# Optimization experiments

Hardware: AMD Instinct MI355X
Metric: run time of the kernel (lower is better)

The kernel has to match this reference:

```python
import jax, jax.numpy as jnp
import numpy as np

H = 1024          # hidden_dim
E = 8             # num_experts
TOP_K = 2
FF = 4 * H        # ExpertFFN inner dim (standard transformer FFN assumption)
B, S = 2, 2048


def setup_inputs() -> dict:
    key = jax.random.key(0)
    ks = jax.random.split(key, 12)
    std = 0.02 / np.sqrt(H)
    return {
        "x": jax.random.normal(ks[0], (B, S, H), dtype=jnp.float32),
        "gate_w": jax.random.normal(ks[1], (E, H), dtype=jnp.float32) * std,  # nn.Linear weight [out,in]
        "gate_b": jnp.zeros((E,), dtype=jnp.float32),                          # self.bias param
        # routed experts, stacked: FFN = W2 @ gelu(W1 @ x + b1) + b2
        "w1": jax.random.normal(ks[2], (E, H, FF), dtype=jnp.float32) * (1.0 / np.sqrt(H)),
        "b1": jnp.zeros((E, FF), dtype=jnp.float32),
        "w2": jax.random.normal(ks[3], (E, FF, H), dtype=jnp.float32) * (1.0 / np.sqrt(FF)),
        "b2": jnp.zeros((E, H), dtype=jnp.float32),
        # shared expert
        "sw1": jax.random.normal(ks[4], (H, FF), dtype=jnp.float32) * (1.0 / np.sqrt(H)),
        "sb1": jnp.zeros((FF,), dtype=jnp.float32),
        "sw2": jax.random.normal(ks[5], (FF, H), dtype=jnp.float32) * (1.0 / np.sqrt(FF)),
        "sb2": jnp.zeros((H,), dtype=jnp.float32),
    }


def _moe_forward(x, gate_w, gate_b, w1, b1, w2, b2, sw1, sb1, sw2, sb2):
    b, s, h = x.shape
    xf = x.reshape(-1, h)                                    # [T, H]
    # sigmoid gating with learned bias (aux-loss-free load balancing bias)
    scores = jax.nn.sigmoid(xf @ gate_w.T + gate_b)          # [T, E]
    top_scores, top_idx = jax.lax.top_k(scores, TOP_K)       # [T, k]
    top_scores = top_scores / (top_scores.sum(-1, keepdims=True) + 1e-6)
    # per-expert combine weights: sum of normalized scores over top-k slots
    comb = (jax.nn.one_hot(top_idx, E, dtype=xf.dtype) * top_scores[..., None]).sum(1)  # [T, E]
    # dense grouped FFN over all experts (reference; faithful math to masked dispatch)
    hdn = jax.nn.gelu(jnp.einsum('th,ehf->etf', xf, w1) + b1[:, None, :], approximate=False)
    y = jnp.einsum('etf,efh->eth', hdn, w2) + b2[:, None, :]  # [E, T, H]
    routed = jnp.einsum('te,eth->th', comb, y)                # [T, H]
    shared = (jax.nn.gelu(xf @ sw1 + sb1, approximate=False) @ sw2 + sb2) * 0.1
    return (routed + shared).reshape(b, s, h)                 # dropout: eval mode (identity)


def reference(x, gate_w, gate_b, w1, b1, w2, b2, sw1, sb1, sw2, sb2):
    return _moe_forward(x, gate_w, gate_b, w1, b1, w2, b2, sw1, sb1, sw2, sb2)
```

## Files before the change

### kernel.cpp

```cpp
#include <hip/hip_runtime.h>
#include <stdint.h>

#define H_DIM 1024
#define E_NUM 8
#define FF_DIM 4096
#define T_TOK 4096
#define MAX_MT 104

typedef __bf16 bf16x8 __attribute__((ext_vector_type(8)));
typedef float f32x4 __attribute__((ext_vector_type(4)));

#define AS1 __attribute__((address_space(1)))
#define AS3 __attribute__((address_space(3)))

__device__ __forceinline__ unsigned short f2bf(float f) {
  union { float f; uint32_t u; } v; v.f = f;
  uint32_t u = v.u;
  uint32_t r = u + 0x7fffu + ((u >> 16) & 1u);
  return (unsigned short)(r >> 16);
}

__device__ __forceinline__ float gelu_f(float x) {
  float s = x * x;
  float g = x * (1.5957691216f + 0.0713548162f * s);
  float t = __expf(-g);
  return x * __builtin_amdgcn_rcpf(1.0f + t);
}

__global__ __launch_bounds__(64) void gate_kernel(
    const float* __restrict__ x, const float* __restrict__ gw, const float* __restrict__ gb,
    int* __restrict__ topidx, float* __restrict__ topw, int* __restrict__ counts) {
  int t = blockIdx.x;
  int l = threadIdx.x;
  const float* xt = x + (size_t)t * H_DIM;
  float acc[E_NUM];
  #pragma unroll
  for (int e = 0; e < E_NUM; e++) acc[e] = 0.f;
  for (int k = l; k < H_DIM; k += 64) {
    float xv = xt[k];
    #pragma unroll
    for (int e = 0; e < E_NUM; e++) acc[e] += xv * gw[e * H_DIM + k];
  }
  #pragma unroll
  for (int e = 0; e < E_NUM; e++) {
    float v = acc[e];
    #pragma unroll
    for (int off = 32; off > 0; off >>= 1) v += __shfl_xor(v, off, 64);
    acc[e] = v;
  }
  if (l == 0) {
    float s[E_NUM];
    #pragma unroll
    for (int e = 0; e < E_NUM; e++) s[e] = 1.f / (1.f + __expf(-(acc[e] + gb[e])));
    int i1 = 0; float v1 = s[0];
    #pragma unroll
    for (int e = 1; e < E_NUM; e++) if (s[e] > v1) { v1 = s[e]; i1 = e; }
    int i2 = -1; float v2 = -1.f;
    #pragma unroll
    for (int e = 0; e < E_NUM; e++) if (e != i1 && s[e] > v2) { v2 = s[e]; i2 = e; }
    float denom = v1 + v2 + 1e-6f;
    topidx[t * 2]     = i1; topidx[t * 2 + 1] = i2;
    topw[t * 2]       = v1 / denom;
    topw[t * 2 + 1]   = v2 / denom;
    atomicAdd(&counts[i1], 1);
    atomicAdd(&counts[i2], 1);
  }
}

__global__ void init_kernel(int* counts) {
  if (threadIdx.x < E_NUM) counts[threadIdx.x] = 0;
}

__global__ void scan_kernel(const int* __restrict__ counts, int* __restrict__ offs,
                            int* __restrict__ cursor, int* __restrict__ tmE,
                            int* __restrict__ tmM, int* __restrict__ tmCnt) {
  if (threadIdx.x == 0) {
    int a = 0;
    for (int e = 0; e < E_NUM; e++) { offs[e] = a; a += counts[e]; cursor[e] = 0; }
    offs[E_NUM] = a;
    offs[E_NUM + 1] = a + T_TOK;
    int c = 0;
    for (int e = 0; e <= E_NUM; e++) {
      int cnt = (e < E_NUM) ? counts[e] : T_TOK;
      for (int m0 = 0; m0 < cnt; m0 += 128) { tmE[c] = e; tmM[c] = m0; c++; }
    }
    tmCnt[0] = c;
  }
}

__global__ void dispatch_kernel(const int* __restrict__ topidx, const float* __restrict__ topw,
                                const int* __restrict__ offs, int* __restrict__ cursor,
                                int* __restrict__ gidx, int* __restrict__ slot_of) {
  int t = blockIdx.x * blockDim.x + threadIdx.x;
  if (t >= T_TOK) return;
  #pragma unroll
  for (int j = 0; j < 2; j++) {
    int ex  = topidx[t * 2 + j];
    int pos = atomicAdd(&cursor[ex], 1);
    int slot = offs[ex] + pos;
    gidx[slot] = t;
    slot_of[t * 2 + j] = slot;
  }
  gidx[2 * T_TOK + t] = t;
}

__global__ __launch_bounds__(256) void cast_x_kernel(const float* __restrict__ x,
                                                     unsigned short* __restrict__ xb) {
  int i = blockIdx.x * blockDim.x + threadIdx.x;
  float4 v = ((const float4*)x)[i];
  ushort4 o;
  o.x = f2bf(v.x); o.y = f2bf(v.y); o.z = f2bf(v.z); o.w = f2bf(v.w);
  ((ushort4*)xb)[i] = o;
}

__global__ __launch_bounds__(256) void transpose_cast_kernel(
    const float* __restrict__ in, unsigned short* __restrict__ out, int R, int C) {
  __shared__ float tile[64][65];
  const size_t bo = (size_t)blockIdx.z * (size_t)R * C;
  const float* inb = in + bo;
  unsigned short* outb = out + bo;
  int c0 = blockIdx.x * 64, r0 = blockIdx.y * 64;
  int tx = threadIdx.x & 15, ty = threadIdx.x >> 4;
  #pragma unroll
  for (int i = 0; i < 4; i++) {
    int row = ty + i * 16;
    float4 v = *(const float4*)(inb + (size_t)(r0 + row) * C + c0 + tx * 4);
    tile[row][tx * 4 + 0] = v.x;
    tile[row][tx * 4 + 1] = v.y;
    tile[row][tx * 4 + 2] = v.z;
    tile[row][tx * 4 + 3] = v.w;
  }
  __syncthreads();
  int rr0 = tx * 4;
  #pragma unroll
  for (int p = 0; p < 4; p++) {
    int col = p * 16 + ty;
    ushort4 o;
    o.x = f2bf(tile[rr0 + 0][col]);
    o.y = f2bf(tile[rr0 + 1][col]);
    o.z = f2bf(tile[rr0 + 2][col]);
    o.w = f2bf(tile[rr0 + 3][col]);
    *(ushort4*)(outb + (size_t)(c0 + col) * R + r0 + rr0) = o;
  }
}

template <bool FFN1>
__global__ __launch_bounds__(256) void gemm128(
    const unsigned short* __restrict__ A,
    const unsigned short* __restrict__ Bt,
    const float* __restrict__ b_r,
    const float* __restrict__ b_s,
    void* __restrict__ outp,
    const int* __restrict__ gidx,
    const int* __restrict__ offs,
    const int* __restrict__ tmE, const int* __restrict__ tmM,
    const int* __restrict__ tmCnt,
    int K, int N) {
  if ((int)blockIdx.y >= tmCnt[0]) return;

  __shared__ __align__(16) char ldsA[128 * 128];
  __shared__ __align__(16) char ldsB[128 * 128];
  __shared__ int tokLds[128];

  const int tid = threadIdx.x;
  const int w = tid >> 6;
  const int l = tid & 63;
  const int e  = tmE[blockIdx.y];
  const int m0 = tmM[blockIdx.y];
  const int cnt = offs[e + 1] - offs[e];
  const int base = offs[e] + m0;
  const int valid = min(128, cnt - m0);
  const int n0 = blockIdx.x * 128;

  if (FFN1) {
    if (tid < 128) tokLds[tid] = gidx[base + min(tid, valid - 1)];
    __syncthreads();
  }

  const int lr = l >> 3;
  const int su = (l & 7) ^ lr;
  const unsigned short* aSrc[4];
  const unsigned short* bSrc[4];
  const unsigned short* BtE = Bt + (size_t)e * (size_t)N * (size_t)K;
  #pragma unroll
  for (int i = 0; i < 4; i++) {
    int r = w * 32 + i * 8 + lr;
    size_t arow = FFN1 ? (size_t)tokLds[r] : (size_t)(base + r);
    aSrc[i] = A + arow * (size_t)K + su * 8;
    int rr = r & 63;
    int nr = n0 + (r & 64) + ((rr & 15) << 2) + (rr >> 4);
    bSrc[i] = BtE + (size_t)nr * (size_t)K + su * 8;
  }
  char* aDst[4];
  char* bDst[4];
  #pragma unroll
  for (int i = 0; i < 4; i++) {
    aDst[i] = ldsA + (w * 32 + i * 8) * 128;
    bDst[i] = ldsB + (w * 32 + i * 8) * 128;
  }

  f32x4 acc[4][4];
  #pragma unroll
  for (int m = 0; m < 4; m++)
    #pragma unroll
    for (int n = 0; n < 4; n++) acc[m][n] = (f32x4){0.f, 0.f, 0.f, 0.f};

  const int wr = w >> 1, wc = w & 1;
  const int l15 = l & 15, l4 = l >> 4, l7 = l & 7;

  for (int kt = 0; kt < K; kt += 64) {
    #pragma unroll
    for (int i = 0; i < 4; i++)
      __builtin_amdgcn_global_load_lds((const AS1 void*)(aSrc[i] + kt),
                                       (AS3 void*)aDst[i], 16, 0, 0);
    #pragma unroll
    for (int i = 0; i < 4; i++)
      __builtin_amdgcn_global_load_lds((const AS1 void*)(bSrc[i] + kt),
                                       (AS3 void*)bDst[i], 16, 0, 0);
    __syncthreads();
    #pragma unroll
    for (int kk = 0; kk < 2; kk++) {
      bf16x8 af[4], bfr[4];
      #pragma unroll
      for (int m = 0; m < 4; m++) {
        int r = wr * 64 + m * 16 + l15;
        af[m] = *(const bf16x8*)(ldsA + r * 128 + (((kk * 4 + l4) ^ l7) << 4));
      }
      #pragma unroll
      for (int n = 0; n < 4; n++) {
        int r = wc * 64 + n * 16 + l15;
        bfr[n] = *(const bf16x8*)(ldsB + r * 128 + (((kk * 4 + l4) ^ l7) << 4));
      }
      #pragma unroll
      for (int m = 0; m < 4; m++)
        #pragma unroll
        for (int n = 0; n < 4; n++)
          acc[m][n] = __builtin_amdgcn_mfma_f32_16x16x32_bf16(af[m], bfr[n], acc[m][n], 0, 0, 0);
    }
    __syncthreads();
  }

  const float* bias = (e < E_NUM) ? (b_r + (size_t)e * N) : b_s;
  const int c0 = n0 + wc * 64 + 4 * l15;
  float4 bv = *(const float4*)(bias + c0);
  if (FFN1) {
    unsigned short* hdn = (unsigned short*)outp;
    #pragma unroll
    for (int m = 0; m < 4; m++) {
      #pragma unroll
      for (int j = 0; j < 4; j++) {
        int rl = wr * 64 + m * 16 + l4 * 4 + j;
        if (rl < valid) {
          ushort4 o;
          o.x = f2bf(gelu_f(acc[m][0][j] + bv.x));
          o.y = f2bf(gelu_f(acc[m][1][j] + bv.y));
          o.z = f2bf(gelu_f(acc[m][2][j] + bv.z));
          o.w = f2bf(gelu_f(acc[m][3][j] + bv.w));
          *(ushort4*)(hdn + (size_t)(base + rl) * N + c0) = o;
        }
      }
    }
  } else {
    float* y = (float*)outp;
    #pragma unroll
    for (int m = 0; m < 4; m++) {
      #pragma unroll
      for (int j = 0; j < 4; j++) {
        int rl = wr * 64 + m * 16 + l4 * 4 + j;
        if (rl < valid) {
          float4 o;
          o.x = acc[m][0][j] + bv.x;
          o.y = acc[m][1][j] + bv.y;
          o.z = acc[m][2][j] + bv.z;
          o.w = acc[m][3][j] + bv.w;
          *(float4*)(y + (size_t)(base + rl) * N + c0) = o;
        }
      }
    }
  }
}

__global__ __launch_bounds__(256) void combine_kernel(
    const float* __restrict__ y, const float* __restrict__ topw,
    const int* __restrict__ slot_of, float* __restrict__ out) {
  int t = blockIdx.x;
  int g = threadIdx.x;
  int s1 = slot_of[2 * t], s2 = slot_of[2 * t + 1];
  float w1 = topw[2 * t], w2 = topw[2 * t + 1];
  float4 a = *(const float4*)(y + (size_t)s1 * H_DIM + g * 4);
  float4 b = *(const float4*)(y + (size_t)s2 * H_DIM + g * 4);
  float4 c = *(const float4*)(y + (size_t)(2 * T_TOK + t) * H_DIM + g * 4);
  float4 o;
  o.x = w1 * a.x + w2 * b.x + 0.1f * c.x;
  o.y = w1 * a.y + w2 * b.y + 0.1f * c.y;
  o.z = w1 * a.z + w2 * b.z + 0.1f * c.z;
  o.w = w1 * a.w + w2 * b.w + 0.1f * c.w;
  *(float4*)(out + (size_t)t * H_DIM + g * 4) = o;
}

extern "C" void kernel_launch(void* const* d_in, const int* in_sizes, int n_in,
                              void* d_out, int out_size, void* d_ws, size_t ws_size,
                              hipStream_t stream) {
  const float* x   = (const float*)d_in[0];
  const float* gw  = (const float*)d_in[1];
  const float* gb  = (const float*)d_in[2];
  const float* w1  = (const float*)d_in[3];
  const float* b1  = (const float*)d_in[4];
  const float* w2  = (const float*)d_in[5];
  const float* b2  = (const float*)d_in[6];
  const float* sw1 = (const float*)d_in[7];
  const float* sb1 = (const float*)d_in[8];
  const float* sw2 = (const float*)d_in[9];
  const float* sb2 = (const float*)d_in[10];
  float* out = (float*)d_out;

  char* p = (char*)d_ws;
  auto alloc = [&](size_t bytes) {
    char* r = p;
    p += (bytes + 255) & ~(size_t)255;
    return r;
  };
  int*   counts  = (int*)alloc(E_NUM * 4);
  int*   cursor  = (int*)alloc(E_NUM * 4);
  int*   offs    = (int*)alloc((E_NUM + 2) * 4);
  int*   topidx  = (int*)alloc((size_t)T_TOK * 2 * 4);
  float* topw    = (float*)alloc((size_t)T_TOK * 2 * 4);
  int*   slot_of = (int*)alloc((size_t)T_TOK * 2 * 4);
  int*   gidx    = (int*)alloc((size_t)3 * T_TOK * 4);
  int*   tmE     = (int*)alloc(MAX_MT * 4);
  int*   tmM     = (int*)alloc(MAX_MT * 4);
  int*   tmCnt   = (int*)alloc(4);
  unsigned short* xb   = (unsigned short*)alloc((size_t)T_TOK * H_DIM * 2);
  unsigned short* wAll = (unsigned short*)alloc((size_t)(E_NUM + 1) * FF_DIM * H_DIM * 2);
  unsigned short* hdn  = (unsigned short*)alloc((size_t)3 * T_TOK * FF_DIM * 2);
  float*          yb   = (float*)alloc((size_t)3 * T_TOK * H_DIM * 4);

  init_kernel<<<1, 64, 0, stream>>>(counts);
  gate_kernel<<<T_TOK, 64, 0, stream>>>(x, gw, gb, topidx, topw, counts);
  scan_kernel<<<1, 1, 0, stream>>>(counts, offs, cursor, tmE, tmM, tmCnt);
  dispatch_kernel<<<T_TOK / 256, 256, 0, stream>>>(topidx, topw, offs, cursor, gidx, slot_of);

  cast_x_kernel<<<(T_TOK * H_DIM / 4) / 256, 256, 0, stream>>>(x, xb);

  transpose_cast_kernel<<<dim3(FF_DIM / 64, H_DIM / 64, E_NUM), 256, 0, stream>>>(w1, wAll, H_DIM, FF_DIM);
  transpose_cast_kernel<<<dim3(FF_DIM / 64, H_DIM / 64, 1), 256, 0, stream>>>(
      sw1, wAll + (size_t)E_NUM * FF_DIM * H_DIM, H_DIM, FF_DIM);
  gemm128<true><<<dim3(FF_DIM / 128, MAX_MT), 256, 0, stream>>>(
      xb, wAll, b1, sb1, hdn, gidx, offs, tmE, tmM, tmCnt, H_DIM, FF_DIM);

  transpose_cast_kernel<<<dim3(H_DIM / 64, FF_DIM / 64, E_NUM), 256, 0, stream>>>(w2, wAll, FF_DIM, H_DIM);
  transpose_cast_kernel<<<dim3(H_DIM / 64, FF_DIM / 64, 1), 256, 0, stream>>>(
      sw2, wAll + (size_t)E_NUM * FF_DIM * H_DIM, FF_DIM, H_DIM);
  gemm128<false><<<dim3(H_DIM / 128, MAX_MT), 256, 0, stream>>>(
      hdn, wAll, b2, sb2, yb, gidx, offs, tmE, tmM, tmCnt, FF_DIM, H_DIM);

  combine_kernel<<<T_TOK, 256, 0, stream>>>(yb, topw, slot_of, out);
}
```

Before: 591.1 us.

## Enlarge grouped GEMM M-tile from 128 to 256 rows per block

Doubles the M dimension of each expert GEMM tile to 256 rows, so each wave computes 128x64 outputs with 8x4 accumulator fragments and reuses B fragments across two A halves. This halves the number of M tiles and the B-weight reloads per output, raising arithmetic intensity. In exchange it doubles the accumulator registers and A LDS use, which may lower occupancy. It also adds more padding waste for experts whose token counts are not multiples of 256, and the FFN2 grid becomes small (8 x 56 blocks).

```diff
diff --git a/kernel.cpp b/kernel.cpp
--- a/kernel.cpp
+++ b/kernel.cpp
@@ -5,7 +5,7 @@
 #define E_NUM 8
 #define FF_DIM 4096
 #define T_TOK 4096
-#define MAX_MT 104
+#define MAX_MT 56
 
 typedef __bf16 bf16x8 __attribute__((ext_vector_type(8)));
 typedef float f32x4 __attribute__((ext_vector_type(4)));
@@ -82,7 +82,7 @@
     int c = 0;
     for (int e = 0; e <= E_NUM; e++) {
       int cnt = (e < E_NUM) ? counts[e] : T_TOK;
-      for (int m0 = 0; m0 < cnt; m0 += 128) { tmE[c] = e; tmM[c] = m0; c++; }
+      for (int m0 = 0; m0 < cnt; m0 += 256) { tmE[c] = e; tmM[c] = m0; c++; }
     }
     tmCnt[0] = c;
   }
@@ -145,7 +145,7 @@
 }
 
 template <bool FFN1>
-__global__ __launch_bounds__(256) void gemm128(
+__global__ __launch_bounds__(256) void gemm256(
     const unsigned short* __restrict__ A,
     const unsigned short* __restrict__ Bt,
     const float* __restrict__ b_r,
@@ -158,9 +158,9 @@
     int K, int N) {
   if ((int)blockIdx.y >= tmCnt[0]) return;
 
-  __shared__ __align__(16) char ldsA[128 * 128];
+  __shared__ __align__(16) char ldsA[256 * 128];
   __shared__ __align__(16) char ldsB[128 * 128];
-  __shared__ int tokLds[128];
+  __shared__ int tokLds[256];
 
   const int tid = threadIdx.x;
   const int w = tid >> 6;
@@ -169,39 +169,42 @@
   const int m0 = tmM[blockIdx.y];
   const int cnt = offs[e + 1] - offs[e];
   const int base = offs[e] + m0;
-  const int valid = min(128, cnt - m0);
+  const int valid = min(256, cnt - m0);
   const int n0 = blockIdx.x * 128;
 
   if (FFN1) {
-    if (tid < 128) tokLds[tid] = gidx[base + min(tid, valid - 1)];
+    tokLds[tid] = gidx[base + min(tid, valid - 1)];
     __syncthreads();
   }
 
-  const int lr = l >> 3;
-  const int su = (l & 7) ^ lr;
-  const unsigned short* aSrc[4];
+  const int lr8 = (tid >> 3) & 7;
+  const int su  = (tid & 7) ^ lr8;
+  const unsigned short* aSrc[8];
   const unsigned short* bSrc[4];
   const unsigned short* BtE = Bt + (size_t)e * (size_t)N * (size_t)K;
   #pragma unroll
-  for (int i = 0; i < 4; i++) {
-    int r = w * 32 + i * 8 + lr;
+  for (int j = 0; j < 8; j++) {
+    int r = j * 32 + (tid >> 3);
     size_t arow = FFN1 ? (size_t)tokLds[r] : (size_t)(base + r);
-    aSrc[i] = A + arow * (size_t)K + su * 8;
+    aSrc[j] = A + arow * (size_t)K + su * 8;
+  }
+  #pragma unroll
+  for (int j = 0; j < 4; j++) {
+    int r = j * 32 + (tid >> 3);
     int rr = r & 63;
     int nr = n0 + (r & 64) + ((rr & 15) << 2) + (rr >> 4);
-    bSrc[i] = BtE + (size_t)nr * (size_t)K + su * 8;
-  }
-  char* aDst[4];
+    bSrc[j] = BtE + (size_t)nr * (size_t)K + su * 8;
+  }
+  char* aDst[8];
   char* bDst[4];
   #pragma unroll
-  for (int i = 0; i < 4; i++) {
-    aDst[i] = ldsA + (w * 32 + i * 8) * 128;
-    bDst[i] = ldsB + (w * 32 + i * 8) * 128;
-  }
-
-  f32x4 acc[4][4];
-  #pragma unroll
-  for (int m = 0; m < 4; m++)
+  for (int j = 0; j < 8; j++) aDst[j] = ldsA + (j * 32 + w * 8) * 128;
+  #pragma unroll
+  for (int j = 0; j < 4; j++) bDst[j] = ldsB + (j * 32 + w * 8) * 128;
+
+  f32x4 acc[8][4];
+  #pragma unroll
+  for (int m = 0; m < 8; m++)
     #pragma unroll
     for (int n = 0; n < 4; n++) acc[m][n] = (f32x4){0.f, 0.f, 0.f, 0.f};
 
@@ -210,32 +213,34 @@
 
   for (int kt = 0; kt < K; kt += 64) {
     #pragma unroll
-    for (int i = 0; i < 4; i++)
-      __builtin_amdgcn_global_load_lds((const AS1 void*)(aSrc[i] + kt),
-                                       (AS3 void*)aDst[i], 16, 0, 0);
-    #pragma unroll
-    for (int i = 0; i < 4; i++)
-      __builtin_amdgcn_global_load_lds((const AS1 void*)(bSrc[i] + kt),
-                                       (AS3 void*)bDst[i], 16, 0, 0);
+    for (int j = 0; j < 8; j++)
+      __builtin_amdgcn_global_load_lds((const AS1 void*)(aSrc[j] + kt),
+                                       (AS3 void*)aDst[j], 16, 0, 0);
+    #pragma unroll
+    for (int j = 0; j < 4; j++)
+      __builtin_amdgcn_global_load_lds((const AS1 void*)(bSrc[j] + kt),
+                                       (AS3 void*)bDst[j], 16, 0, 0);
     __syncthreads();
     #pragma unroll
     for (int kk = 0; kk < 2; kk++) {
-      bf16x8 af[4], bfr[4];
+      const int uoff = ((kk * 4 + l4) ^ l7) << 4;
+      bf16x8 bfr[4];
       #pragma unroll
-      for (int m = 0; m < 4; m++) {
-        int r = wr * 64 + m * 16 + l15;
-        af[m] = *(const bf16x8*)(ldsA + r * 128 + (((kk * 4 + l4) ^ l7) << 4));
+      for (int n = 0; n < 4; n++)
+        bfr[n] = *(const bf16x8*)(ldsB + (wc * 64 + n * 16 + l15) * 128 + uoff);
+      #pragma unroll
+      for (int mh = 0; mh < 2; mh++) {
+        bf16x8 af[4];
+        #pragma unroll
+        for (int m = 0; m < 4; m++)
+          af[m] = *(const bf16x8*)(ldsA + (wr * 128 + (mh * 4 + m) * 16 + l15) * 128 + uoff);
+        #pragma unroll
+        for (int m = 0; m < 4; m++)
+          #pragma unroll
+          for (int n = 0; n < 4; n++)
+            acc[mh * 4 + m][n] = __builtin_amdgcn_mfma_f32_16x16x32_bf16(
+                af[m], bfr[n], acc[mh * 4 + m][n], 0, 0, 0);
       }
-      #pragma unroll
-      for (int n = 0; n < 4; n++) {
-        int r = wc * 64 + n * 16 + l15;
-        bfr[n] = *(const bf16x8*)(ldsB + r * 128 + (((kk * 4 + l4) ^ l7) << 4));
-      }
-      #pragma unroll
-      for (int m = 0; m < 4; m++)
-        #pragma unroll
-        for (int n = 0; n < 4; n++)
-          acc[m][n] = __builtin_amdgcn_mfma_f32_16x16x32_bf16(af[m], bfr[n], acc[m][n], 0, 0, 0);
     }
     __syncthreads();
   }
@@ -246,16 +251,16 @@
   if (FFN1) {
     unsigned short* hdn = (unsigned short*)outp;
     #pragma unroll
-    for (int m = 0; m < 4; m++) {
+    for (int fm = 0; fm < 8; fm++) {
       #pragma unroll
       for (int j = 0; j < 4; j++) {
-        int rl = wr * 64 + m * 16 + l4 * 4 + j;
+        int rl = wr * 128 + fm * 16 + l4 * 4 + j;
         if (rl < valid) {
           ushort4 o;
-          o.x = f2bf(gelu_f(acc[m][0][j] + bv.x));
-          o.y = f2bf(gelu_f(acc[m][1][j] + bv.y));
-          o.z = f2bf(gelu_f(acc[m][2][j] + bv.z));
-          o.w = f2bf(gelu_f(acc[m][3][j] + bv.w));
+          o.x = f2bf(gelu_f(acc[fm][0][j] + bv.x));
+          o.y = f2bf(gelu_f(acc[fm][1][j] + bv.y));
+          o.z = f2bf(gelu_f(acc[fm][2][j] + bv.z));
+          o.w = f2bf(gelu_f(acc[fm][3][j] + bv.w));
           *(ushort4*)(hdn + (size_t)(base + rl) * N + c0) = o;
         }
       }
@@ -263,16 +268,16 @@
   } else {
     float* y = (float*)outp;
     #pragma unroll
-    for (int m = 0; m < 4; m++) {
+    for (int fm = 0; fm < 8; fm++) {
       #pragma unroll
       for (int j = 0; j < 4; j++) {
-        int rl = wr * 64 + m * 16 + l4 * 4 + j;
+        int rl = wr * 128 + fm * 16 + l4 * 4 + j;
         if (rl < valid) {
           float4 o;
-          o.x = acc[m][0][j] + bv.x;
-          o.y = acc[m][1][j] + bv.y;
-          o.z = acc[m][2][j] + bv.z;
-          o.w = acc[m][3][j] + bv.w;
+          o.x = acc[fm][0][j] + bv.x;
+          o.y = acc[fm][1][j] + bv.y;
+          o.z = acc[fm][2][j] + bv.z;
+          o.w = acc[fm][3][j] + bv.w;
           *(float4*)(y + (size_t)(base + rl) * N + c0) = o;
         }
       }
@@ -345,13 +350,13 @@
   transpose_cast_kernel<<<dim3(FF_DIM / 64, H_DIM / 64, E_NUM), 256, 0, stream>>>(w1, wAll, H_DIM, FF_DIM);
   transpose_cast_kernel<<<dim3(FF_DIM / 64, H_DIM / 64, 1), 256, 0, stream>>>(
       sw1, wAll + (size_t)E_NUM * FF_DIM * H_DIM, H_DIM, FF_DIM);
-  gemm128<true><<<dim3(FF_DIM / 128, MAX_MT), 256, 0, stream>>>(
+  gemm256<true><<<dim3(FF_DIM / 128, MAX_MT), 256, 0, stream>>>(
       xb, wAll, b1, sb1, hdn, gidx, offs, tmE, tmM, tmCnt, H_DIM, FF_DIM);
 
   transpose_cast_kernel<<<dim3(H_DIM / 64, FF_DIM / 64, E_NUM), 256, 0, stream>>>(w2, wAll, FF_DIM, H_DIM);
   transpose_cast_kernel<<<dim3(H_DIM / 64, FF_DIM / 64, 1), 256, 0, stream>>>(
       sw2, wAll + (size_t)E_NUM * FF_DIM * H_DIM, FF_DIM, H_DIM);
-  gemm128<false><<<dim3(H_DIM / 128, MAX_MT), 256, 0, stream>>>(
+  gemm256<false><<<dim3(H_DIM / 128, MAX_MT), 256, 0, stream>>>(
       hdn, wAll, b2, sb2, yb, gidx, offs, tmE, tmM, tmCnt, FF_DIM, H_DIM);
 
   combine_kernel<<<T_TOK, 256, 0, stream>>>(yb, topw, slot_of, out);
```

New measurement: 755.7 us. 27.9% more time.

## Double-buffer LDS tiles to overlap global loads with MFMA compute

Applied to the files above, without the earlier changes.

The grouped GEMM kernel now keeps two LDS buffers for the A and B tiles and issues the global-to-LDS loads for the next K-step before computing on the current one. The aim is to hide global memory latency behind the MFMA work instead of stalling on a barrier after every load. LDS use per block doubles to about 64KB, which may lower occupancy. There is one barrier per iteration, and correctness depends on that barrier, together with the vmcnt wait the compiler inserts before it, ordering the asynchronous LDS writes.

```diff
diff --git a/kernel.cpp b/kernel.cpp
--- a/kernel.cpp
+++ b/kernel.cpp
@@ -158,8 +158,8 @@
     int K, int N) {
   if ((int)blockIdx.y >= tmCnt[0]) return;
 
-  __shared__ __align__(16) char ldsA[128 * 128];
-  __shared__ __align__(16) char ldsB[128 * 128];
+  __shared__ __align__(16) char ldsA[2][128 * 128];
+  __shared__ __align__(16) char ldsB[2][128 * 128];
   __shared__ int tokLds[128];
 
   const int tid = threadIdx.x;
@@ -191,12 +191,19 @@
     int nr = n0 + (r & 64) + ((rr & 15) << 2) + (rr >> 4);
     bSrc[i] = BtE + (size_t)nr * (size_t)K + su * 8;
   }
-  char* aDst[4];
-  char* bDst[4];
-  #pragma unroll
-  for (int i = 0; i < 4; i++) {
-    aDst[i] = ldsA + (w * 32 + i * 8) * 128;
-    bDst[i] = ldsB + (w * 32 + i * 8) * 128;
+  const int dOff = (w * 32 + lr) * 128;
+
+#define STAGE(c, kt)                                                               \
+  {                                                                                \
+    _Pragma("unroll")                                                              \
+    for (int i = 0; i < 4; i++) {                                                  \
+      __builtin_amdgcn_global_load_lds((const AS1 void*)(aSrc[i] + (kt) * 64),     \
+                                       (AS3 void*)(&ldsA[c][i * 1024 + dOff]),     \
+                                       16, 0, 0);                                  \
+      __builtin_amdgcn_global_load_lds((const AS1 void*)(bSrc[i] + (kt) * 64),     \
+                                       (AS3 void*)(&ldsB[c][i * 1024 + dOff]),     \
+                                       16, 0, 0);                                  \
+    }                                                                              \
   }
 
   f32x4 acc[4][4];
@@ -207,30 +214,27 @@
 
   const int wr = w >> 1, wc = w & 1;
   const int l15 = l & 15, l4 = l >> 4, l7 = l & 7;
-
-  for (int kt = 0; kt < K; kt += 64) {
-    #pragma unroll
-    for (int i = 0; i < 4; i++)
-      __builtin_amdgcn_global_load_lds((const AS1 void*)(aSrc[i] + kt),
-                                       (AS3 void*)aDst[i], 16, 0, 0);
-    #pragma unroll
-    for (int i = 0; i < 4; i++)
-      __builtin_amdgcn_global_load_lds((const AS1 void*)(bSrc[i] + kt),
-                                       (AS3 void*)bDst[i], 16, 0, 0);
-    __syncthreads();
+  const int nt = K >> 6;
+
+  STAGE(0, 0);
+  __syncthreads();
+
+  for (int t = 0; t < nt; t++) {
+    const int cur = t & 1;
+    if (t + 1 < nt) STAGE(cur ^ 1, t + 1);
+
+    const char* pA = &ldsA[cur][0];
+    const char* pB = &ldsB[cur][0];
     #pragma unroll
     for (int kk = 0; kk < 2; kk++) {
+      const int uoff = ((kk * 4 + l4) ^ l7) << 4;
       bf16x8 af[4], bfr[4];
       #pragma unroll
-      for (int m = 0; m < 4; m++) {
-        int r = wr * 64 + m * 16 + l15;
-        af[m] = *(const bf16x8*)(ldsA + r * 128 + (((kk * 4 + l4) ^ l7) << 4));
-      }
-      #pragma unroll
-      for (int n = 0; n < 4; n++) {
-        int r = wc * 64 + n * 16 + l15;
-        bfr[n] = *(const bf16x8*)(ldsB + r * 128 + (((kk * 4 + l4) ^ l7) << 4));
-      }
+      for (int m = 0; m < 4; m++)
+        af[m] = *(const bf16x8*)(pA + (wr * 64 + m * 16 + l15) * 128 + uoff);
+      #pragma unroll
+      for (int n = 0; n < 4; n++)
+        bfr[n] = *(const bf16x8*)(pB + (wc * 64 + n * 16 + l15) * 128 + uoff);
       #pragma unroll
       for (int m = 0; m < 4; m++)
         #pragma unroll
@@ -239,6 +243,7 @@
     }
     __syncthreads();
   }
+#undef STAGE
 
   const float* bias = (e < E_NUM) ? (b_r + (size_t)e * N) : b_s;
   const int c0 = n0 + wc * 64 + 4 * l15;
```

New measurement: 594.6 us. Within noise of the previous version (+0.6%).
